# Performance work log

Hardware: AMD Instinct MI355X
Metric: run time of the kernel (lower is better)

The kernel has to match this reference:

```python
import jax, jax.numpy as jnp
import numpy as np

B, S, I, H = 64, 1024, 256, 256


def setup_inputs() -> dict:
    key = jax.random.key(0)
    ks = jax.random.split(key, 20)
    k = (1.0 / H) ** 0.5
    u = lambda kk, shape: jax.random.uniform(kk, shape, jnp.float32, -k, k)
    inp = {
        'inputs': jax.random.normal(ks[0], (B, S, I), jnp.float32),
        'h0': jax.random.normal(ks[1], (1, B, H), jnp.float32),
        'c0': jax.random.normal(ks[2], (1, B, H), jnp.float32),
        'w_ii': u(ks[3], (H, I)), 'w_if': u(ks[4], (H, I)),
        'w_ig': u(ks[5], (H, I)), 'w_io': u(ks[6], (H, I)),
        'b_ii': u(ks[7], (H,)), 'b_if': u(ks[8], (H,)),
        'b_ig': u(ks[9], (H,)), 'b_io': u(ks[10], (H,)),
        'w_hi': u(ks[11], (H, H)), 'w_hf': u(ks[12], (H, H)),
        'w_hg': u(ks[13], (H, H)), 'w_ho': u(ks[14], (H, H)),
        'b_hi': u(ks[15], (H,)), 'b_hf': u(ks[16], (H,)),
        'b_hg': u(ks[17], (H,)), 'b_ho': u(ks[18], (H,)),
    }
    return inp


def reference(inputs, h0, c0, w_ii, w_if, w_ig, w_io, b_ii, b_if, b_ig, b_io,
              w_hi, w_hf, w_hg, w_ho, b_hi, b_hf, b_hg, b_ho):
    # Precompute all input-to-gate projections over the whole sequence (one big GEMM each).
    # Shapes: [B, S, H] -> transposed to [S, B, H] for the time scan.
    xi = (jnp.einsum('bsi,hi->bsh', inputs, w_ii) + b_ii + b_hi).transpose(1, 0, 2)
    xf = (jnp.einsum('bsi,hi->bsh', inputs, w_if) + b_if + b_hf).transpose(1, 0, 2)
    xg = (jnp.einsum('bsi,hi->bsh', inputs, w_ig) + b_ig + b_hg).transpose(1, 0, 2)
    xo = (jnp.einsum('bsi,hi->bsh', inputs, w_io) + b_io + b_ho).transpose(1, 0, 2)

    def step(carry, xs):
        h, c = carry  # [B, H] each
        xi_t, xf_t, xg_t, xo_t = xs
        i_t = jax.nn.sigmoid(xi_t + h @ w_hi.T)
        f_t = jax.nn.sigmoid(xf_t + h @ w_hf.T)
        g_t = jnp.tanh(xg_t + h @ w_hg.T)
        o_t = jax.nn.sigmoid(xo_t + h @ w_ho.T)
        c = f_t * c + i_t * g_t
        h = o_t * jnp.tanh(c)
        return (h, c), h

    (hN, cN), hs = jax.lax.scan(step, (h0[0], c0[0]), (xi, xf, xg, xo))
    x = hs.transpose(1, 0, 2)  # [B, S, H]
    return x, (hN[None], cN[None])
```

## Files before the change

### kernel.cpp

```cpp
#include <hip/hip_runtime.h>
#include <hip/hip_fp16.h>
#include <stdint.h>


typedef __attribute__((ext_vector_type(4))) int v4i;
typedef __attribute__((ext_vector_type(4))) float f32x4;
typedef __attribute__((ext_vector_type(8))) short short8;
typedef __attribute__((ext_vector_type(2))) unsigned u32x2;

#define S_LEN 1024
#define HID 256
#define NB 64
#define PA 68
#define HP 288

__device__ __forceinline__ short f2bf(float f) {
  union { float f; unsigned u; } v; v.f = f;
  unsigned r = v.u + 0x7FFFu + ((v.u >> 16) & 1u);
  return (short)(r >> 16);
}

__device__ __forceinline__ float fsigm(float x) {
  return __builtin_amdgcn_rcpf(1.0f + __expf(-x));
}
__device__ __forceinline__ float ftanh(float x) {
  return 2.0f * __builtin_amdgcn_rcpf(1.0f + __expf(-2.0f * x)) - 1.0f;
}

__global__ __launch_bounds__(256) void conv_bf16(
    const float* __restrict__ inputs,
    const float* __restrict__ w_ii, const float* __restrict__ w_if,
    const float* __restrict__ w_ig, const float* __restrict__ w_io,
    unsigned short* __restrict__ Abf, unsigned short* __restrict__ Wbf) {
  const size_t NIN8 = (size_t)NB * S_LEN * HID / 8;
  const size_t NW8 = (size_t)4 * HID * HID / 8;
  size_t i = (size_t)blockIdx.x * 256 + threadIdx.x;
  const float* src;
  unsigned short* dst;
  if (i < NIN8) {
    src = inputs + i * 8;
    dst = Abf + i * 8;
  } else if (i < NIN8 + NW8) {
    size_t w8 = i - NIN8;
    int g = (int)(w8 >> 13);
    const float* Wg = (g == 0) ? w_ii : (g == 1) ? w_if : (g == 2) ? w_ig : w_io;
    src = Wg + (w8 & 8191) * 8;
    dst = Wbf + w8 * 8;
  } else {
    return;
  }
  float4 a = ((const float4*)src)[0];
  float4 b = ((const float4*)src)[1];
  union { short s[8]; short8 v; } pk;
  pk.s[0] = f2bf(a.x); pk.s[1] = f2bf(a.y); pk.s[2] = f2bf(a.z); pk.s[3] = f2bf(a.w);
  pk.s[4] = f2bf(b.x); pk.s[5] = f2bf(b.y); pk.s[6] = f2bf(b.z); pk.s[7] = f2bf(b.w);
  *(short8*)dst = pk.v;
}

__global__ __launch_bounds__(256) void lstm_xproj(
    const unsigned short* __restrict__ Abf, const unsigned short* __restrict__ Wbf,
    const float* __restrict__ b_ii, const float* __restrict__ b_if,
    const float* __restrict__ b_ig, const float* __restrict__ b_io,
    const float* __restrict__ b_hi, const float* __restrict__ b_hf,
    const float* __restrict__ b_hg, const float* __restrict__ b_ho,
    unsigned short* __restrict__ xacc, int t0, int TC) {
  __shared__ short lds[2 * 128 * PA];
  short* Alds = lds;
  short* Blds = lds + 128 * PA;
  unsigned short* Osh = (unsigned short*)lds;

  const int tid = threadIdx.x;
  const int bx = blockIdx.x;
  const int jtgp = blockIdx.y;
  const int grp = blockIdx.z;

  const int wv = tid >> 6;
  const int lane = tid & 63;
  const int jl = lane & 15;
  const int kg = lane >> 4;

  const int R = tid >> 1;
  const int half = tid & 1;
  const int bloc = R & 15;
  const int tloc_s = R >> 4;

  const unsigned short* asrc = Abf +
      ((size_t)(grp * 16 + bloc) * S_LEN + (t0 + bx * 8 + tloc_s)) * HID + half * 32;
  const int cS = R;
  const unsigned short* bsrc = Wbf +
      ((size_t)((cS & 3) * HID + jtgp * 32 + (cS >> 2))) * HID + half * 32;

  f32x4 acc[2][8];
#pragma unroll
  for (int ms = 0; ms < 2; ++ms)
#pragma unroll
    for (int ct = 0; ct < 8; ++ct) acc[ms][ct] = (f32x4){0, 0, 0, 0};

  for (int ks = 0; ks < HID; ks += 64) {
    __syncthreads();
    short8 av[4], bv[4];
#pragma unroll
    for (int i = 0; i < 4; ++i) {
      av[i] = *(const short8*)(asrc + ks + i * 8);
      bv[i] = *(const short8*)(bsrc + ks + i * 8);
    }
#pragma unroll
    for (int i = 0; i < 4; ++i) {
      *(short8*)&Alds[R * PA + half * 32 + i * 8] = av[i];
      *(short8*)&Blds[R * PA + half * 32 + i * 8] = bv[i];
    }
    __syncthreads();
#pragma unroll
    for (int kk = 0; kk < 2; ++kk) {
      short8 af0 = *(const short8*)&Alds[((wv * 2 + 0) * 16 + jl) * PA + kk * 32 + kg * 8];
      short8 af1 = *(const short8*)&Alds[((wv * 2 + 1) * 16 + jl) * PA + kk * 32 + kg * 8];
#pragma unroll
      for (int ct = 0; ct < 8; ++ct) {
        short8 bf = *(const short8*)&Blds[(ct * 16 + jl) * PA + kk * 32 + kg * 8];
        acc[0][ct] = __builtin_amdgcn_mfma_f32_16x16x32_bf16(af0, bf, acc[0][ct], 0, 0, 0);
        acc[1][ct] = __builtin_amdgcn_mfma_f32_16x16x32_bf16(af1, bf, acc[1][ct], 0, 0, 0);
      }
    }
  }

  const int g = jl & 3;
  const float* B1g = (g == 0) ? b_ii : (g == 1) ? b_if : (g == 2) ? b_ig : b_io;
  const float* B2g = (g == 0) ? b_hi : (g == 1) ? b_hf : (g == 2) ? b_hg : b_ho;
  float bias[8];
#pragma unroll
  for (int ct = 0; ct < 8; ++ct) {
    int j = jtgp * 32 + ct * 4 + (jl >> 2);
    bias[ct] = B1g[j] + B2g[j];
  }

  __syncthreads();
#pragma unroll
  for (int ms = 0; ms < 2; ++ms) {
    const int tloc = wv * 2 + ms;
#pragma unroll
    for (int ct = 0; ct < 8; ++ct) {
      int jloc = ct * 4 + (jl >> 2);
      int cb = ((jloc >> 4) << 10) + (jloc & 15) * 16 + kg * 256 + (jl & 3);
#pragma unroll
      for (int ri = 0; ri < 4; ++ri) {
        float v = acc[ms][ct][ri] + bias[ct];
        Osh[tloc * 2048 + cb + ri * 4] = __half_as_ushort(__float2half(v));
      }
    }
  }
  __syncthreads();

#pragma unroll
  for (int t2 = 0; t2 < 8; ++t2) {
    int tl = bx * 8 + t2;
    *(short8*)(xacc + (((size_t)(tl * 4 + grp)) << 14) + jtgp * 2048 + tid * 8) =
        *(const short8*)&Osh[t2 * 2048 + tid * 8];
  }
}

__global__ __launch_bounds__(1024) void lstm_scan(
    const float* __restrict__ h0, const float* __restrict__ c0,
    const float* __restrict__ w_hi, const float* __restrict__ w_hf,
    const float* __restrict__ w_hg, const float* __restrict__ w_ho,
    float* __restrict__ out, const unsigned short* __restrict__ xacc,
    unsigned* __restrict__ ws_h8, float* __restrict__ ws_c,
    int t0, int TC) {
  __shared__ char h8[2][4 * HP];

  const int tid = threadIdx.x;
  const int jt = tid >> 6;
  const int lane = tid & 63;
  const int jl = lane & 15;
  const int kg = lane >> 4;
  const int ngrp = blockIdx.x;
  const int b = ngrp * 4 + kg;
  const int jc = jt * 16 + jl;

  const float* Wg4[4] = {w_hi, w_hf, w_hg, w_ho};
  v4i W8[16];
#pragma unroll
  for (int g = 0; g < 4; ++g) {
#pragma unroll
    for (int w = 0; w < 4; ++w) {
      const float4* p = (const float4*)(Wg4[g] +
          (size_t)jc * HID + w * 64 + kg * 16);
      int bb[16];
#pragma unroll
      for (int q = 0; q < 4; ++q) {
        float4 v = p[q];
        bb[q*4+0] = (int)fminf(fmaxf(rintf(v.x * 2032.f), -127.f), 127.f);
        bb[q*4+1] = (int)fminf(fmaxf(rintf(v.y * 2032.f), -127.f), 127.f);
        bb[q*4+2] = (int)fminf(fmaxf(rintf(v.z * 2032.f), -127.f), 127.f);
        bb[q*4+3] = (int)fminf(fmaxf(rintf(v.w * 2032.f), -127.f), 127.f);
      }
      v4i pk;
#pragma unroll
      for (int q = 0; q < 4; ++q)
        pk[q] = (bb[q*4+0] & 255) | ((bb[q*4+1] & 255) << 8) |
                ((bb[q*4+2] & 255) << 16) | ((bb[q*4+3] & 255) << 24);
      W8[g * 4 + w] = pk;
    }
  }

  float c;
  if (t0 == 0) c = c0[(size_t)b * HID + jc];
  else         c = ws_c[(size_t)b * HID + jc];

  if (t0 == 0) {
    if (tid < 256) {
      int row = tid >> 6;
      int cc = (tid & 63) * 4;
      float4 hv = *(const float4*)(h0 + (size_t)(ngrp * 4 + row) * HID + cc);
      int b0 = (int)fminf(fmaxf(rintf(hv.x * 31.75f), -127.f), 127.f);
      int b1 = (int)fminf(fmaxf(rintf(hv.y * 31.75f), -127.f), 127.f);
      int b2 = (int)fminf(fmaxf(rintf(hv.z * 31.75f), -127.f), 127.f);
      int b3 = (int)fminf(fmaxf(rintf(hv.w * 31.75f), -127.f), 127.f);
      *(int*)&h8[0][row * HP + cc] =
          (b0 & 255) | ((b1 & 255) << 8) | ((b2 & 255) << 16) | ((b3 & 255) << 24);
    }
  } else {
    if (tid < 256)
      *(unsigned*)&h8[t0 & 1][(tid >> 6) * HP + (tid & 63) * 4] =
          ws_h8[ngrp * 256 + tid];
  }
  __syncthreads();

  const float qn = 1.0f / (127.f * 2032.f);
  const float q0 = 1.0f / (31.75f * 2032.f);

  const unsigned short* xp = xacc + ((size_t)(ngrp >> 2) << 14) +
      (size_t)((jt * 64 + jl + ((ngrp & 3) << 4)) * 16 + kg * 4);
  float* outp = out + ((size_t)b * S_LEN + t0) * HID + jc;

  const int arow = (jl >> 2) * HP;

  for (int t = t0; t < t0 + TC; ++t) {
    const int cur = t & 1;
    const int nxt = cur ^ 1;

    u32x2 xv = *(const u32x2*)xp;
    xp += 65536;

    v4i acc[4];
#pragma unroll
    for (int g = 0; g < 4; ++g) acc[g] = (v4i){0, 0, 0, 0};
#pragma unroll
    for (int w = 0; w < 4; ++w) {
      v4i a = *(const v4i*)&h8[cur][arow + w * 64 + kg * 16];
#pragma unroll
      for (int g = 0; g < 4; ++g)
        acc[g] = __builtin_amdgcn_mfma_i32_16x16x64_i8(a, W8[g * 4 + w], acc[g], 0, 0, 0);
    }

    const float q = (t == 0) ? q0 : qn;
    const __half* xh = (const __half*)&xv;
    float pre_i = (float)acc[0][0] * q + __half2float(xh[0]);
    float pre_f = (float)acc[1][0] * q + __half2float(xh[1]);
    float pre_g = (float)acc[2][0] * q + __half2float(xh[2]);
    float pre_o = (float)acc[3][0] * q + __half2float(xh[3]);
    float iv = fsigm(pre_i);
    float fv = fsigm(pre_f);
    float gv = ftanh(pre_g);
    float ov = fsigm(pre_o);
    c = fv * c + iv * gv;
    float hh = ov * ftanh(c);

    *outp = hh;
    outp += HID;
    if (t == S_LEN - 1) {
      out[(size_t)NB * S_LEN * HID + (size_t)b * HID + jc] = hh;
      out[(size_t)NB * S_LEN * HID + (size_t)NB * HID + (size_t)b * HID + jc] = c;
    }
    int q8 = (int)fminf(fmaxf(rintf(hh * 127.f), -127.f), 127.f);
    h8[nxt][kg * HP + jc] = (char)q8;
    __syncthreads();
  }

  if (tid < 256)
    ws_h8[ngrp * 256 + tid] =
        *(const unsigned*)&h8[(t0 + TC) & 1][(tid >> 6) * HP + (tid & 63) * 4];
  ws_c[(size_t)b * HID + jc] = c;
}

extern "C" void kernel_launch(void* const* d_in, const int* in_sizes, int n_in,
                              void* d_out, int out_size, void* d_ws, size_t ws_size,
                              hipStream_t stream) {
  const float* inputs = (const float*)d_in[0];
  const float* h0 = (const float*)d_in[1];
  const float* c0 = (const float*)d_in[2];
  const float* w_ii = (const float*)d_in[3];
  const float* w_if = (const float*)d_in[4];
  const float* w_ig = (const float*)d_in[5];
  const float* w_io = (const float*)d_in[6];
  const float* b_ii = (const float*)d_in[7];
  const float* b_if = (const float*)d_in[8];
  const float* b_ig = (const float*)d_in[9];
  const float* b_io = (const float*)d_in[10];
  const float* w_hi = (const float*)d_in[11];
  const float* w_hf = (const float*)d_in[12];
  const float* w_hg = (const float*)d_in[13];
  const float* w_ho = (const float*)d_in[14];
  const float* b_hi = (const float*)d_in[15];
  const float* b_hf = (const float*)d_in[16];
  const float* b_hg = (const float*)d_in[17];
  const float* b_ho = (const float*)d_in[18];

  float* out = (float*)d_out;

  const size_t wb = (size_t)4 * HID * HID * 2;
  const size_t ab = (size_t)NB * S_LEN * HID * 2;
  const size_t base = wb + ab + 32768 + 65536;

  unsigned short* Wbf = (unsigned short*)d_ws;
  unsigned short* Abf = (unsigned short*)((char*)d_ws + wb);
  unsigned* ws_h8 = (unsigned*)((char*)d_ws + wb + ab);
  float* ws_c = (float*)((char*)d_ws + wb + ab + 32768);
  unsigned short* xacc = (unsigned short*)((char*)d_ws + base);

  int TC = 64;
  const int cands[5] = {1024, 512, 256, 128, 64};
  for (int i = 0; i < 5; ++i) {
    size_t need = base + (size_t)cands[i] * 131072;
    if (need <= ws_size) { TC = cands[i]; break; }
  }

  conv_bf16<<<8320, 256, 0, stream>>>(inputs, w_ii, w_if, w_ig, w_io, Abf, Wbf);

  for (int t0 = 0; t0 < S_LEN; t0 += TC) {
    lstm_xproj<<<dim3(TC / 8, 8, 4), 256, 0, stream>>>(
        Abf, Wbf,
        b_ii, b_if, b_ig, b_io, b_hi, b_hf, b_hg, b_ho,
        xacc, t0, TC);
    lstm_scan<<<16, 1024, 0, stream>>>(
        h0, c0, w_hi, w_hf, w_hg, w_ho,
        out, xacc, ws_h8, ws_c, t0, TC);
  }
}
```

Baseline: 1.298 ms.

## Fuse input projection and recurrent scan into one producer-consumer kernel

Adds a single persistent kernel in which 16 blocks run the recurrent LSTM scan while 240 blocks compute the bf16 input-projection GEMM. Producers signal per-8-timestep completion via atomic counters and the scan blocks spin-wait on them, so the projection overlaps the serial recurrence instead of running before it in separate launches. The scan keeps int8-quantized recurrent weights in registers and uses int8 MFMA. The fused path is taken only when the workspace fits the full sequence. It relies on all blocks being co-resident to avoid deadlock and adds spin-wait and atomic overhead.

```diff
diff --git a/kernel.cpp b/kernel.cpp
--- a/kernel.cpp
+++ b/kernel.cpp
@@ -12,7 +12,9 @@
 #define HID 256
 #define NB 64
 #define PA 68
+#define PF 36
 #define HP 288
+#define NXB 240
 
 __device__ __forceinline__ short f2bf(float f) {
   union { float f; unsigned u; } v; v.f = f;
@@ -57,6 +59,230 @@
   *(short8*)dst = pk.v;
 }
 
+__global__ __launch_bounds__(1024) void lstm_fused(
+    const unsigned short* __restrict__ Abf, const unsigned short* __restrict__ Wbf,
+    const float* __restrict__ b_ii, const float* __restrict__ b_if,
+    const float* __restrict__ b_ig, const float* __restrict__ b_io,
+    const float* __restrict__ b_hi, const float* __restrict__ b_hf,
+    const float* __restrict__ b_hg, const float* __restrict__ b_ho,
+    const float* __restrict__ h0, const float* __restrict__ c0,
+    const float* __restrict__ w_hi, const float* __restrict__ w_hf,
+    const float* __restrict__ w_hg, const float* __restrict__ w_ho,
+    float* __restrict__ out, unsigned short* __restrict__ xacc,
+    unsigned* __restrict__ cnt) {
+  __shared__ __align__(16) char smem[46080];
+
+  const int tid = threadIdx.x;
+  const int lane = tid & 63;
+  const int jl = lane & 15;
+  const int kg = lane >> 4;
+
+  if (blockIdx.x < 16) {
+    const int jt = tid >> 6;
+    const int ngrp = blockIdx.x;
+    const int b = ngrp * 4 + kg;
+    const int jc = jt * 16 + jl;
+
+    char (*h8)[4 * HP] = (char (*)[4 * HP])smem;
+
+    const float* Wg4[4] = {w_hi, w_hf, w_hg, w_ho};
+    v4i W8[16];
+#pragma unroll
+    for (int g = 0; g < 4; ++g) {
+#pragma unroll
+      for (int w = 0; w < 4; ++w) {
+        const float4* p = (const float4*)(Wg4[g] +
+            (size_t)jc * HID + w * 64 + kg * 16);
+        int bb[16];
+#pragma unroll
+        for (int q = 0; q < 4; ++q) {
+          float4 v = p[q];
+          bb[q*4+0] = (int)fminf(fmaxf(rintf(v.x * 2032.f), -127.f), 127.f);
+          bb[q*4+1] = (int)fminf(fmaxf(rintf(v.y * 2032.f), -127.f), 127.f);
+          bb[q*4+2] = (int)fminf(fmaxf(rintf(v.z * 2032.f), -127.f), 127.f);
+          bb[q*4+3] = (int)fminf(fmaxf(rintf(v.w * 2032.f), -127.f), 127.f);
+        }
+        v4i pk;
+#pragma unroll
+        for (int q = 0; q < 4; ++q)
+          pk[q] = (bb[q*4+0] & 255) | ((bb[q*4+1] & 255) << 8) |
+                  ((bb[q*4+2] & 255) << 16) | ((bb[q*4+3] & 255) << 24);
+        W8[g * 4 + w] = pk;
+      }
+    }
+
+    float c = c0[(size_t)b * HID + jc];
+
+    if (tid < 256) {
+      int row = tid >> 6;
+      int cc = (tid & 63) * 4;
+      float4 hv = *(const float4*)(h0 + (size_t)(ngrp * 4 + row) * HID + cc);
+      int b0 = (int)fminf(fmaxf(rintf(hv.x * 31.75f), -127.f), 127.f);
+      int b1 = (int)fminf(fmaxf(rintf(hv.y * 31.75f), -127.f), 127.f);
+      int b2 = (int)fminf(fmaxf(rintf(hv.z * 31.75f), -127.f), 127.f);
+      int b3 = (int)fminf(fmaxf(rintf(hv.w * 31.75f), -127.f), 127.f);
+      *(int*)&h8[0][row * HP + cc] =
+          (b0 & 255) | ((b1 & 255) << 8) | ((b2 & 255) << 16) | ((b3 & 255) << 24);
+    }
+    __syncthreads();
+
+    const float qn = 1.0f / (127.f * 2032.f);
+    const float q0 = 1.0f / (31.75f * 2032.f);
+
+    const unsigned short* xp = xacc + (((size_t)(ngrp >> 2)) << 14) +
+        (size_t)((jt * 64 + jl + ((ngrp & 3) << 4)) * 16 + kg * 4);
+    float* outp = out + (size_t)b * S_LEN * HID + jc;
+    const int arow = (jl >> 2) * HP;
+
+    for (int t = 0; t < S_LEN; ++t) {
+      if ((t & 7) == 0) {
+        if (tid == 0) {
+          while (__hip_atomic_load(cnt + (t >> 3), __ATOMIC_ACQUIRE,
+                                   __HIP_MEMORY_SCOPE_AGENT) < 8u)
+            __builtin_amdgcn_s_sleep(8);
+        }
+        __syncthreads();
+        __builtin_amdgcn_fence(__ATOMIC_ACQUIRE, "agent");
+      }
+      const int cur = t & 1;
+      const int nxt = cur ^ 1;
+
+      u32x2 xv = *(const u32x2*)xp;
+      xp += 65536;
+
+      v4i acc[4];
+#pragma unroll
+      for (int g = 0; g < 4; ++g) acc[g] = (v4i){0, 0, 0, 0};
+#pragma unroll
+      for (int w = 0; w < 4; ++w) {
+        v4i a = *(const v4i*)&h8[cur][arow + w * 64 + kg * 16];
+#pragma unroll
+        for (int g = 0; g < 4; ++g)
+          acc[g] = __builtin_amdgcn_mfma_i32_16x16x64_i8(a, W8[g * 4 + w], acc[g], 0, 0, 0);
+      }
+
+      const float q = (t == 0) ? q0 : qn;
+      const __half* xh = (const __half*)&xv;
+      float pre_i = (float)acc[0][0] * q + __half2float(xh[0]);
+      float pre_f = (float)acc[1][0] * q + __half2float(xh[1]);
+      float pre_g = (float)acc[2][0] * q + __half2float(xh[2]);
+      float pre_o = (float)acc[3][0] * q + __half2float(xh[3]);
+      float iv = fsigm(pre_i);
+      float fv = fsigm(pre_f);
+      float gv = ftanh(pre_g);
+      float ov = fsigm(pre_o);
+      c = fv * c + iv * gv;
+      float hh = ov * ftanh(c);
+
+      *outp = hh;
+      outp += HID;
+      if (t == S_LEN - 1) {
+        out[(size_t)NB * S_LEN * HID + (size_t)b * HID + jc] = hh;
+        out[(size_t)NB * S_LEN * HID + (size_t)NB * HID + (size_t)b * HID + jc] = c;
+      }
+      int q8 = (int)fminf(fmaxf(rintf(hh * 127.f), -127.f), 127.f);
+      h8[nxt][kg * HP + jc] = (char)q8;
+      __syncthreads();
+    }
+  } else {
+    const int p0 = (int)blockIdx.x - 16;
+    const int sub = tid >> 8;
+    const int stid = tid & 255;
+    const int wv = (tid >> 6) & 3;
+
+    short* As = (short*)smem;
+    short* Bs = (short*)smem + 128 * PF + sub * 128 * PF;
+    unsigned short* Osh = (unsigned short*)smem + sub * 4096;
+
+    const int R = stid >> 1;
+    const int half = stid & 1;
+
+    for (int item = p0; item < 1024; item += NXB) {
+      const int bx = item >> 3;
+      const int rr = item & 7;
+      const int grp = rr >> 1;
+      const int jtgp = (rr & 1) * 4 + sub;
+
+      const unsigned short* asrc = Abf +
+          ((size_t)(grp * 16 + (R & 15)) * S_LEN + bx * 8 + (R >> 4)) * HID + half * 16;
+      const unsigned short* bsrc = Wbf +
+          ((size_t)((R & 3) * HID + jtgp * 32 + (R >> 2))) * HID + half * 16;
+
+      f32x4 acc[2][8];
+#pragma unroll
+      for (int ms = 0; ms < 2; ++ms)
+#pragma unroll
+        for (int ct = 0; ct < 8; ++ct) acc[ms][ct] = (f32x4){0, 0, 0, 0};
+
+      for (int ks = 0; ks < 8; ++ks) {
+        __syncthreads();
+        short8 bv0 = *(const short8*)(bsrc + ks * 32);
+        short8 bv1 = *(const short8*)(bsrc + ks * 32 + 8);
+        short8 av0, av1;
+        if (sub == 0) {
+          av0 = *(const short8*)(asrc + ks * 32);
+          av1 = *(const short8*)(asrc + ks * 32 + 8);
+        }
+        *(short8*)&Bs[R * PF + half * 16] = bv0;
+        *(short8*)&Bs[R * PF + half * 16 + 8] = bv1;
+        if (sub == 0) {
+          *(short8*)&As[R * PF + half * 16] = av0;
+          *(short8*)&As[R * PF + half * 16 + 8] = av1;
+        }
+        __syncthreads();
+
+        short8 af0 = *(const short8*)&As[((wv * 2 + 0) * 16 + jl) * PF + kg * 8];
+        short8 af1 = *(const short8*)&As[((wv * 2 + 1) * 16 + jl) * PF + kg * 8];
+#pragma unroll
+        for (int ct = 0; ct < 8; ++ct) {
+          short8 bf = *(const short8*)&Bs[(ct * 16 + jl) * PF + kg * 8];
+          acc[0][ct] = __builtin_amdgcn_mfma_f32_16x16x32_bf16(af0, bf, acc[0][ct], 0, 0, 0);
+          acc[1][ct] = __builtin_amdgcn_mfma_f32_16x16x32_bf16(af1, bf, acc[1][ct], 0, 0, 0);
+        }
+      }
+
+      const int g = jl & 3;
+      const float* B1g = (g == 0) ? b_ii : (g == 1) ? b_if : (g == 2) ? b_ig : b_io;
+      const float* B2g = (g == 0) ? b_hi : (g == 1) ? b_hf : (g == 2) ? b_hg : b_ho;
+      float bias[8];
+#pragma unroll
+      for (int ct = 0; ct < 8; ++ct) {
+        int j = jtgp * 32 + ct * 4 + (jl >> 2);
+        bias[ct] = B1g[j] + B2g[j];
+      }
+
+      for (int tq = 0; tq < 4; ++tq) {
+        __syncthreads();
+        if (wv == tq) {
+#pragma unroll
+          for (int ms = 0; ms < 2; ++ms) {
+#pragma unroll
+            for (int ct = 0; ct < 8; ++ct) {
+              int jloc = ct * 4 + (jl >> 2);
+              int cb = ((jloc >> 4) << 10) + (jloc & 15) * 16 + kg * 256 + (jl & 3);
+#pragma unroll
+              for (int ri = 0; ri < 4; ++ri) {
+                float v = acc[ms][ct][ri] + bias[ct];
+                Osh[ms * 2048 + cb + ri * 4] = __half_as_ushort(__float2half(v));
+              }
+            }
+          }
+        }
+        __syncthreads();
+#pragma unroll
+        for (int t2 = 0; t2 < 2; ++t2) {
+          int tl = bx * 8 + tq * 2 + t2;
+          *(short8*)(xacc + (((size_t)(tl * 4 + grp)) << 14) + jtgp * 2048 + stid * 8) =
+              *(const short8*)&Osh[t2 * 2048 + stid * 8];
+        }
+      }
+      __syncthreads();
+      if (tid == 0)
+        __hip_atomic_fetch_add(cnt + bx, 1u, __ATOMIC_RELEASE, __HIP_MEMORY_SCOPE_AGENT);
+    }
+  }
+}
+
 __global__ __launch_bounds__(256) void lstm_xproj(
     const unsigned short* __restrict__ Abf, const unsigned short* __restrict__ Wbf,
     const float* __restrict__ b_ii, const float* __restrict__ b_if,
@@ -81,14 +307,11 @@
 
   const int R = tid >> 1;
   const int half = tid & 1;
-  const int bloc = R & 15;
-  const int tloc_s = R >> 4;
 
   const unsigned short* asrc = Abf +
-      ((size_t)(grp * 16 + bloc) * S_LEN + (t0 + bx * 8 + tloc_s)) * HID + half * 32;
-  const int cS = R;
+      ((size_t)(grp * 16 + (R & 15)) * S_LEN + (t0 + bx * 8 + (R >> 4))) * HID + half * 32;
   const unsigned short* bsrc = Wbf +
-      ((size_t)((cS & 3) * HID + jtgp * 32 + (cS >> 2))) * HID + half * 32;
+      ((size_t)((R & 3) * HID + jtgp * 32 + (R >> 2))) * HID + half * 32;
 
   f32x4 acc[2][8];
 #pragma unroll
@@ -309,12 +532,13 @@
 
   const size_t wb = (size_t)4 * HID * HID * 2;
   const size_t ab = (size_t)NB * S_LEN * HID * 2;
-  const size_t base = wb + ab + 32768 + 65536;
+  const size_t base = wb + ab + 32768 + 65536 + 1024;
 
   unsigned short* Wbf = (unsigned short*)d_ws;
   unsigned short* Abf = (unsigned short*)((char*)d_ws + wb);
   unsigned* ws_h8 = (unsigned*)((char*)d_ws + wb + ab);
   float* ws_c = (float*)((char*)d_ws + wb + ab + 32768);
+  unsigned* cnt = (unsigned*)((char*)d_ws + wb + ab + 32768 + 65536);
   unsigned short* xacc = (unsigned short*)((char*)d_ws + base);
 
   int TC = 64;
@@ -326,13 +550,22 @@
 
   conv_bf16<<<8320, 256, 0, stream>>>(inputs, w_ii, w_if, w_ig, w_io, Abf, Wbf);
 
-  for (int t0 = 0; t0 < S_LEN; t0 += TC) {
-    lstm_xproj<<<dim3(TC / 8, 8, 4), 256, 0, stream>>>(
+  if (TC == 1024) {
+    hipMemsetAsync(cnt, 0, 128 * sizeof(unsigned), stream);
+    lstm_fused<<<16 + NXB, 1024, 0, stream>>>(
         Abf, Wbf,
         b_ii, b_if, b_ig, b_io, b_hi, b_hf, b_hg, b_ho,
-        xacc, t0, TC);
-    lstm_scan<<<16, 1024, 0, stream>>>(
         h0, c0, w_hi, w_hf, w_hg, w_ho,
-        out, xacc, ws_h8, ws_c, t0, TC);
-  }
-}
+        out, xacc, cnt);
+  } else {
+    for (int t0 = 0; t0 < S_LEN; t0 += TC) {
+      lstm_xproj<<<dim3(TC / 8, 8, 4), 256, 0, stream>>>(
+          Abf, Wbf,
+          b_ii, b_if, b_ig, b_io, b_hi, b_hf, b_hg, b_ho,
+          xacc, t0, TC);
+      lstm_scan<<<16, 1024, 0, stream>>>(
+          h0, c0, w_hi, w_hf, w_hg, w_ho,
+          out, xacc, ws_h8, ws_c, t0, TC);
+    }
+  }
+}
```

Result: slower. 1.373 ms (+5.8%).

## Give each batch row its own scan block with a 256-thread MFMA recurrence

Applied to the files above, without the earlier changes.

The recurrent scan kernel now runs 64 blocks of 256 threads, one block per batch element, instead of 16 blocks of 1024 threads covering four batches each. Each wave keeps four times more int8 weight tiles in registers and issues 64 MFMAs per step. Only one of the 16 MFMA output rows is useful (the broadcast h row), and the result is picked out with lane selects. The x-projection kernel's output layout is rearranged to match the new per-batch indexing. The goal is to spread the latency-bound serial scan across more CUs and to use cheaper 256-thread barriers, at the cost of redundant MFMA work and much higher register pressure per thread.

```diff
diff --git a/kernel.cpp b/kernel.cpp
--- a/kernel.cpp
+++ b/kernel.cpp
@@ -12,7 +12,6 @@
 #define HID 256
 #define NB 64
 #define PA 68
-#define HP 288
 
 __device__ __forceinline__ short f2bf(float f) {
   union { float f; unsigned u; } v; v.f = f;
@@ -81,14 +80,11 @@
 
   const int R = tid >> 1;
   const int half = tid & 1;
-  const int bloc = R & 15;
-  const int tloc_s = R >> 4;
 
   const unsigned short* asrc = Abf +
-      ((size_t)(grp * 16 + bloc) * S_LEN + (t0 + bx * 8 + tloc_s)) * HID + half * 32;
-  const int cS = R;
+      ((size_t)(grp * 16 + (R & 15)) * S_LEN + (t0 + bx * 8 + (R >> 4))) * HID + half * 32;
   const unsigned short* bsrc = Wbf +
-      ((size_t)((cS & 3) * HID + jtgp * 32 + (cS >> 2))) * HID + half * 32;
+      ((size_t)((R & 3) * HID + jtgp * 32 + (R >> 2))) * HID + half * 32;
 
   f32x4 acc[2][8];
 #pragma unroll
@@ -140,99 +136,96 @@
 #pragma unroll
     for (int ct = 0; ct < 8; ++ct) {
       int jloc = ct * 4 + (jl >> 2);
-      int cb = ((jloc >> 4) << 10) + (jloc & 15) * 16 + kg * 256 + (jl & 3);
 #pragma unroll
       for (int ri = 0; ri < 4; ++ri) {
+        int bloc = kg * 4 + ri;
         float v = acc[ms][ct][ri] + bias[ct];
-        Osh[tloc * 2048 + cb + ri * 4] = __half_as_ushort(__float2half(v));
+        Osh[tloc * 2048 + bloc * 128 + jloc * 4 + g] =
+            __half_as_ushort(__float2half(v));
       }
     }
   }
   __syncthreads();
 
+  const int bloc_s = tid >> 4;
+  const int off_s = (tid & 15) * 8;
 #pragma unroll
   for (int t2 = 0; t2 < 8; ++t2) {
     int tl = bx * 8 + t2;
-    *(short8*)(xacc + (((size_t)(tl * 4 + grp)) << 14) + jtgp * 2048 + tid * 8) =
-        *(const short8*)&Osh[t2 * 2048 + tid * 8];
-  }
-}
-
-__global__ __launch_bounds__(1024) void lstm_scan(
+    *(short8*)(xacc + (((size_t)(tl * 64 + grp * 16 + bloc_s)) << 10) +
+               jtgp * 128 + off_s) =
+        *(const short8*)&Osh[t2 * 2048 + bloc_s * 128 + off_s];
+  }
+}
+
+__global__ __launch_bounds__(256, 1) void lstm_scan(
     const float* __restrict__ h0, const float* __restrict__ c0,
     const float* __restrict__ w_hi, const float* __restrict__ w_hf,
     const float* __restrict__ w_hg, const float* __restrict__ w_ho,
     float* __restrict__ out, const unsigned short* __restrict__ xacc,
-    unsigned* __restrict__ ws_h8, float* __restrict__ ws_c,
+    unsigned char* __restrict__ ws_h8, float* __restrict__ ws_c,
     int t0, int TC) {
-  __shared__ char h8[2][4 * HP];
+  __shared__ char h8[2][256];
 
   const int tid = threadIdx.x;
   const int jt = tid >> 6;
   const int lane = tid & 63;
   const int jl = lane & 15;
   const int kg = lane >> 4;
-  const int ngrp = blockIdx.x;
-  const int b = ngrp * 4 + kg;
-  const int jc = jt * 16 + jl;
+  const int nb = blockIdx.x;
+  const int col = jt * 64 + lane;
 
   const float* Wg4[4] = {w_hi, w_hf, w_hg, w_ho};
-  v4i W8[16];
-#pragma unroll
-  for (int g = 0; g < 4; ++g) {
-#pragma unroll
-    for (int w = 0; w < 4; ++w) {
-      const float4* p = (const float4*)(Wg4[g] +
-          (size_t)jc * HID + w * 64 + kg * 16);
-      int bb[16];
-#pragma unroll
-      for (int q = 0; q < 4; ++q) {
-        float4 v = p[q];
-        bb[q*4+0] = (int)fminf(fmaxf(rintf(v.x * 2032.f), -127.f), 127.f);
-        bb[q*4+1] = (int)fminf(fmaxf(rintf(v.y * 2032.f), -127.f), 127.f);
-        bb[q*4+2] = (int)fminf(fmaxf(rintf(v.z * 2032.f), -127.f), 127.f);
-        bb[q*4+3] = (int)fminf(fmaxf(rintf(v.w * 2032.f), -127.f), 127.f);
+  v4i W8[4][4][4];
+#pragma unroll
+  for (int tt = 0; tt < 4; ++tt) {
+#pragma unroll
+    for (int g = 0; g < 4; ++g) {
+#pragma unroll
+      for (int w = 0; w < 4; ++w) {
+        const float4* p = (const float4*)(Wg4[g] +
+            (size_t)(jt * 64 + tt * 16 + jl) * HID + w * 64 + kg * 16);
+        int bb[16];
+#pragma unroll
+        for (int q = 0; q < 4; ++q) {
+          float4 v = p[q];
+          bb[q*4+0] = (int)fminf(fmaxf(rintf(v.x * 2032.f), -127.f), 127.f);
+          bb[q*4+1] = (int)fminf(fmaxf(rintf(v.y * 2032.f), -127.f), 127.f);
+          bb[q*4+2] = (int)fminf(fmaxf(rintf(v.z * 2032.f), -127.f), 127.f);
+          bb[q*4+3] = (int)fminf(fmaxf(rintf(v.w * 2032.f), -127.f), 127.f);
+        }
+        v4i pk;
+#pragma unroll
+        for (int q = 0; q < 4; ++q)
+          pk[q] = (bb[q*4+0] & 255) | ((bb[q*4+1] & 255) << 8) |
+                  ((bb[q*4+2] & 255) << 16) | ((bb[q*4+3] & 255) << 24);
+        W8[tt][g][w] = pk;
       }
-      v4i pk;
-#pragma unroll
-      for (int q = 0; q < 4; ++q)
-        pk[q] = (bb[q*4+0] & 255) | ((bb[q*4+1] & 255) << 8) |
-                ((bb[q*4+2] & 255) << 16) | ((bb[q*4+3] & 255) << 24);
-      W8[g * 4 + w] = pk;
     }
   }
 
   float c;
-  if (t0 == 0) c = c0[(size_t)b * HID + jc];
-  else         c = ws_c[(size_t)b * HID + jc];
+  if (t0 == 0) c = c0[(size_t)nb * HID + col];
+  else         c = ws_c[(size_t)nb * HID + col];
 
   if (t0 == 0) {
-    if (tid < 256) {
-      int row = tid >> 6;
-      int cc = (tid & 63) * 4;
-      float4 hv = *(const float4*)(h0 + (size_t)(ngrp * 4 + row) * HID + cc);
-      int b0 = (int)fminf(fmaxf(rintf(hv.x * 31.75f), -127.f), 127.f);
-      int b1 = (int)fminf(fmaxf(rintf(hv.y * 31.75f), -127.f), 127.f);
-      int b2 = (int)fminf(fmaxf(rintf(hv.z * 31.75f), -127.f), 127.f);
-      int b3 = (int)fminf(fmaxf(rintf(hv.w * 31.75f), -127.f), 127.f);
-      *(int*)&h8[0][row * HP + cc] =
-          (b0 & 255) | ((b1 & 255) << 8) | ((b2 & 255) << 16) | ((b3 & 255) << 24);
-    }
+    float hv = h0[(size_t)nb * HID + col];
+    int q8 = (int)fminf(fmaxf(rintf(hv * 31.75f), -127.f), 127.f);
+    h8[0][col] = (char)q8;
   } else {
-    if (tid < 256)
-      *(unsigned*)&h8[t0 & 1][(tid >> 6) * HP + (tid & 63) * 4] =
-          ws_h8[ngrp * 256 + tid];
+    h8[t0 & 1][col] = (char)ws_h8[nb * 256 + col];
   }
   __syncthreads();
 
   const float qn = 1.0f / (127.f * 2032.f);
   const float q0 = 1.0f / (31.75f * 2032.f);
 
-  const unsigned short* xp = xacc + ((size_t)(ngrp >> 2) << 14) +
-      (size_t)((jt * 64 + jl + ((ngrp & 3) << 4)) * 16 + kg * 4);
-  float* outp = out + ((size_t)b * S_LEN + t0) * HID + jc;
-
-  const int arow = (jl >> 2) * HP;
+  const unsigned short* xp = xacc + ((size_t)nb << 10) + col * 4;
+  float* outp = out + ((size_t)nb * S_LEN + t0) * HID + col;
+
+  const int k1 = kg & 1;
+  const int k2 = kg & 2;
+  const v4i z4 = {0, 0, 0, 0};
 
   for (int t = t0; t < t0 + TC; ++t) {
     const int cur = t & 1;
@@ -241,23 +234,47 @@
     u32x2 xv = *(const u32x2*)xp;
     xp += 65536;
 
-    v4i acc[4];
-#pragma unroll
-    for (int g = 0; g < 4; ++g) acc[g] = (v4i){0, 0, 0, 0};
-#pragma unroll
-    for (int w = 0; w < 4; ++w) {
-      v4i a = *(const v4i*)&h8[cur][arow + w * 64 + kg * 16];
+    v4i a0 = *(const v4i*)&h8[cur][0 * 64 + kg * 16];
+    v4i a1 = *(const v4i*)&h8[cur][1 * 64 + kg * 16];
+    v4i a2 = *(const v4i*)&h8[cur][2 * 64 + kg * 16];
+    v4i a3 = *(const v4i*)&h8[cur][3 * 64 + kg * 16];
+
+    v4i acc[4][4];
+#pragma unroll
+    for (int tt = 0; tt < 4; ++tt)
 #pragma unroll
       for (int g = 0; g < 4; ++g)
-        acc[g] = __builtin_amdgcn_mfma_i32_16x16x64_i8(a, W8[g * 4 + w], acc[g], 0, 0, 0);
+        acc[tt][g] = __builtin_amdgcn_mfma_i32_16x16x64_i8(a0, W8[tt][g][0], z4, 0, 0, 0);
+#pragma unroll
+    for (int tt = 0; tt < 4; ++tt)
+#pragma unroll
+      for (int g = 0; g < 4; ++g)
+        acc[tt][g] = __builtin_amdgcn_mfma_i32_16x16x64_i8(a1, W8[tt][g][1], acc[tt][g], 0, 0, 0);
+#pragma unroll
+    for (int tt = 0; tt < 4; ++tt)
+#pragma unroll
+      for (int g = 0; g < 4; ++g)
+        acc[tt][g] = __builtin_amdgcn_mfma_i32_16x16x64_i8(a2, W8[tt][g][2], acc[tt][g], 0, 0, 0);
+#pragma unroll
+    for (int tt = 0; tt < 4; ++tt)
+#pragma unroll
+      for (int g = 0; g < 4; ++g)
+        acc[tt][g] = __builtin_amdgcn_mfma_i32_16x16x64_i8(a3, W8[tt][g][3], acc[tt][g], 0, 0, 0);
+
+    int sel[4];
+#pragma unroll
+    for (int g = 0; g < 4; ++g) {
+      int lo = k1 ? acc[1][g][0] : acc[0][g][0];
+      int hi = k1 ? acc[3][g][0] : acc[2][g][0];
+      sel[g] = k2 ? hi : lo;
     }
 
     const float q = (t == 0) ? q0 : qn;
     const __half* xh = (const __half*)&xv;
-    float pre_i = (float)acc[0][0] * q + __half2float(xh[0]);
-    float pre_f = (float)acc[1][0] * q + __half2float(xh[1]);
-    float pre_g = (float)acc[2][0] * q + __half2float(xh[2]);
-    float pre_o = (float)acc[3][0] * q + __half2float(xh[3]);
+    float pre_i = (float)sel[0] * q + __half2float(xh[0]);
+    float pre_f = (float)sel[1] * q + __half2float(xh[1]);
+    float pre_g = (float)sel[2] * q + __half2float(xh[2]);
+    float pre_o = (float)sel[3] * q + __half2float(xh[3]);
     float iv = fsigm(pre_i);
     float fv = fsigm(pre_f);
     float gv = ftanh(pre_g);
@@ -268,18 +285,16 @@
     *outp = hh;
     outp += HID;
     if (t == S_LEN - 1) {
-      out[(size_t)NB * S_LEN * HID + (size_t)b * HID + jc] = hh;
-      out[(size_t)NB * S_LEN * HID + (size_t)NB * HID + (size_t)b * HID + jc] = c;
+      out[(size_t)NB * S_LEN * HID + (size_t)nb * HID + col] = hh;
+      out[(size_t)NB * S_LEN * HID + (size_t)NB * HID + (size_t)nb * HID + col] = c;
     }
     int q8 = (int)fminf(fmaxf(rintf(hh * 127.f), -127.f), 127.f);
-    h8[nxt][kg * HP + jc] = (char)q8;
+    h8[nxt][col] = (char)q8;
     __syncthreads();
   }
 
-  if (tid < 256)
-    ws_h8[ngrp * 256 + tid] =
-        *(const unsigned*)&h8[(t0 + TC) & 1][(tid >> 6) * HP + (tid & 63) * 4];
-  ws_c[(size_t)b * HID + jc] = c;
+  ws_h8[nb * 256 + col] = (unsigned char)h8[(t0 + TC) & 1][col];
+  ws_c[(size_t)nb * HID + col] = c;
 }
 
 extern "C" void kernel_launch(void* const* d_in, const int* in_sizes, int n_in,
@@ -309,11 +324,11 @@
 
   const size_t wb = (size_t)4 * HID * HID * 2;
   const size_t ab = (size_t)NB * S_LEN * HID * 2;
-  const size_t base = wb + ab + 32768 + 65536;
+  const size_t base = wb + ab + 32768 + 65536 + 1024;
 
   unsigned short* Wbf = (unsigned short*)d_ws;
   unsigned short* Abf = (unsigned short*)((char*)d_ws + wb);
-  unsigned* ws_h8 = (unsigned*)((char*)d_ws + wb + ab);
+  unsigned char* ws_h8 = (unsigned char*)((char*)d_ws + wb + ab);
   float* ws_c = (float*)((char*)d_ws + wb + ab + 32768);
   unsigned short* xacc = (unsigned short*)((char*)d_ws + base);
 
@@ -331,7 +346,7 @@
         Abf, Wbf,
         b_ii, b_if, b_ig, b_io, b_hi, b_hf, b_hg, b_ho,
         xacc, t0, TC);
-    lstm_scan<<<16, 1024, 0, stream>>>(
+    lstm_scan<<<64, 256, 0, stream>>>(
         h0, c0, w_hi, w_hf, w_hg, w_ho,
         out, xacc, ws_h8, ws_c, t0, TC);
   }
```

Measured after the change: 1.507 ms. 16.1% more time.
